# Optimization experiments

Hardware: AMD Instinct MI355X
Metric: run time of the kernel (lower is better)

The kernel has to match this reference:

```python
import jax, jax.numpy as jnp
import numpy as np

VOCAB, EMB, H1, H2, T, B = 21, 128, 64, 100, 500, 1024


def lstm(x, W_ih, W_hh, b_ih, b_hh):
    # x: [B, T, D]; torch gate order i, f, g, o
    Bx, H = x.shape[0], W_hh.shape[1]
    xproj = jnp.einsum('btd,gd->btg', x, W_ih) + b_ih  # [B, T, 4H]

    def step(carry, xt):
        h, c = carry
        gates = xt + h @ W_hh.T + b_hh
        i, f, g, o = jnp.split(gates, 4, axis=-1)
        c = jax.nn.sigmoid(f) * c + jax.nn.sigmoid(i) * jnp.tanh(g)
        h = jax.nn.sigmoid(o) * jnp.tanh(c)
        return (h, c), h

    h0 = jnp.zeros((Bx, H), x.dtype)
    _, hs = jax.lax.scan(step, (h0, h0), xproj.transpose(1, 0, 2))
    return hs.transpose(1, 0, 2)  # [B, T, H]


def setup_inputs() -> dict:
    key = jax.random.key(0)
    ks = jax.random.split(key, 12)
    s = 0.05
    x_idx = jax.random.randint(ks[0], (B, T), 0, VOCAB, dtype=jnp.int32)
    emb_table = jax.random.normal(ks[1], (VOCAB, EMB), jnp.float32) * s
    emb_table = emb_table.at[0].set(0.0)  # padding_idx=0
    d = dict(
        x_idx=x_idx,
        emb_table=emb_table,
        W_ih1=jax.random.normal(ks[2], (4 * H1, EMB), jnp.float32) * s,
        W_hh1=jax.random.normal(ks[3], (4 * H1, H1), jnp.float32) * s,
        b_ih1=jax.random.normal(ks[4], (4 * H1,), jnp.float32) * s,
        b_hh1=jax.random.normal(ks[5], (4 * H1,), jnp.float32) * s,
        W_ih2=jax.random.normal(ks[6], (4 * H2, H1), jnp.float32) * s,
        W_hh2=jax.random.normal(ks[7], (4 * H2, H2), jnp.float32) * s,
        b_ih2=jax.random.normal(ks[8], (4 * H2,), jnp.float32) * s,
        b_hh2=jax.random.normal(ks[9], (4 * H2,), jnp.float32) * s,
        fc_w=jax.random.normal(ks[10], (1, H2), jnp.float32) * s,
        fc_b=jax.random.normal(ks[11], (1,), jnp.float32) * s,
    )
    return d


def reference(x_idx, emb_table, W_ih1, W_hh1, b_ih1, b_hh1,
              W_ih2, W_hh2, b_ih2, b_hh2, fc_w, fc_b):
    # embedding with padding_idx=0 (row is zero; mask keeps grads faithful)
    x = emb_table[x_idx] * (x_idx != 0)[..., None].astype(emb_table.dtype)  # [B,T,128]
    x = lstm(x, W_ih1, W_hh1, b_ih1, b_hh1)  # [B,T,64]
    # MaxPool1d(kernel=5, stride=5) over time
    Bx, Tx, D = x.shape
    Tp = Tx // 5
    x = x[:, :Tp * 5].reshape(Bx, Tp, 5, D).max(axis=2)  # [B,T/5,64]
    x = lstm(x, W_ih2, W_hh2, b_ih2, b_hh2)  # [B,T/5,100]
    h = x[:, -1, :]
    return jax.nn.sigmoid(h @ fc_w.T + fc_b)  # [B,1]
```

## Files before the change

kernel.cpp:

```cpp
#include <hip/hip_runtime.h>

#define VOCAB 21
#define EMB 128
#define H1 64
#define H2 100
#define T1 500
#define TP 100
#define NB 1024
#define TBL_LD 260
#define LOG2E 1.44269504f

typedef __attribute__((ext_vector_type(8))) short bf16x8;
typedef __attribute__((ext_vector_type(4))) float f32x4;

__device__ __forceinline__ unsigned short f2bf(float x){
    union { float f; unsigned u; } v; v.f = x;
    return (unsigned short)((v.u + 0x8000u) >> 16);
}
__device__ __forceinline__ void bar_lds(){
    asm volatile("s_waitcnt lgkmcnt(0)\n\ts_barrier" ::: "memory");
}
__device__ __forceinline__ float ex2(float x){ return __builtin_amdgcn_exp2f(x); }
__device__ __forceinline__ float rcp(float x){ return __builtin_amdgcn_rcpf(x); }

__global__ void k_table(const float* __restrict__ Wih, const float* __restrict__ emb,
                        const float* __restrict__ bih, const float* __restrict__ bhh,
                        float* __restrict__ table){
    const int p = threadIdx.x;
    const int v = blockIdx.x;
    const int orig = (p & 3) * H1 + (p >> 2);
    float s = bih[orig] + bhh[orig];
    if (v != 0){
        const float* w = Wih + orig * EMB;
        const float* e = emb + v * EMB;
        #pragma unroll 16
        for (int d = 0; d < EMB; ++d) s += w[d]*e[d];
    }
    table[v*TBL_LD + p] = s * LOG2E;
}

__global__ __launch_bounds__(1024, 1) void k_lstm1(
    const int* __restrict__ xidx, const float* __restrict__ Whh,
    const float* __restrict__ tbl_g, unsigned short* __restrict__ x2b){
  __shared__ __align__(16) float table[VOCAB*TBL_LD];
  __shared__ __align__(16) unsigned short hbuf[2][16*64];
  __shared__ int idxs[16*T1];

  const int tid = threadIdx.x;
  const int gt = tid >> 6, l = tid & 63;
  const int b0 = blockIdx.x * 16;
  const int row = l & 15, kg = l >> 4;

  for (int i = tid; i < VOCAB*TBL_LD; i += 1024) table[i] = tbl_g[i];
  for (int i = tid; i < 16*T1; i += 1024){
      int r = i / T1, t = i - r*T1;
      idxs[i] = xidx[(b0 + r)*T1 + t];
  }
  { unsigned short* hz = (unsigned short*)hbuf;
    for (int i = tid; i < 2048; i += 1024) hz[i] = 0; }

  bf16x8 af0, af1;
  {
      const int p = 16*gt + row;
      const int orig = (p & 3)*H1 + (p >> 2);
      bf16x8 f;
      const float* s0 = Whh + orig*H1 + kg*8;
      #pragma unroll
      for (int j = 0; j < 8; ++j) f[j] = (short)f2bf(s0[j] * LOG2E);
      af0 = f;
      const float* s1 = Whh + orig*H1 + 32 + kg*8;
      #pragma unroll
      for (int j = 0; j < 8; ++j) f[j] = (short)f2bf(s1[j] * LOG2E);
      af1 = f;
  }

  char* hb = (char*)hbuf;
  const int swz = (row & 7) << 4;
  const int rb0 = (row*128 + 16*kg) ^ swz;
  const int rb1 = (row*128 + 64 + 16*kg) ^ swz;
  const int cell = 4*gt + kg;
  const int wbh  = (row*128 + 2*cell) ^ swz;
  const float twoL = 2.0f * LOG2E;

  float cc = 0.f, pm = -1e30f;
  __syncthreads();

  int vv = idxs[row*T1];
  f32x4 tq = *(const f32x4*)&table[vv*TBL_LD + 4*cell];
  int vnext = idxs[row*T1 + 1];

  int rp = 0, tm = 0, tp = 0;
  for (int t = 0; t < T1; ++t){
      bf16x8 bf0 = *(const bf16x8*)(hb + rp + rb0);
      bf16x8 bf1 = *(const bf16x8*)(hb + rp + rb1);
      f32x4 a = __builtin_amdgcn_mfma_f32_16x16x32_bf16(af0, bf0, tq, 0,0,0);
      f32x4 z = __builtin_amdgcn_mfma_f32_16x16x32_bf16(af1, bf1, a, 0,0,0);
      f32x4 tqn = *(const f32x4*)&table[vnext*TBL_LD + 4*cell];
      int vn2 = idxs[row*T1 + ((t + 2 < T1) ? (t + 2) : 0)];
      float si = rcp(1.f + ex2(-z[0]));
      float sf = rcp(1.f + ex2(-z[1]));
      float so = rcp(1.f + ex2(-z[3]));
      float tg = 1.f - 2.f*rcp(1.f + ex2(z[2] + z[2]));
      cc = sf*cc + si*tg;
      float th = 1.f - 2.f*rcp(1.f + ex2(twoL*cc));
      float h = so*th;
      const int wp = rp ^ 2048;
      *(unsigned short*)(hb + wp + wbh) = f2bf(h);
      pm = fmaxf(pm, h);
      if (++tm == 5){
          x2b[(b0 + row)*(TP*H1) + tp*H1 + cell] = f2bf(pm);
          pm = -1e30f; tm = 0; ++tp;
      }
      tq = tqn; vnext = vn2;
      rp = wp;
      bar_lds();
  }
}

__global__ __launch_bounds__(512, 1) void k_lstm2(
    const unsigned short* __restrict__ x2b, const float* __restrict__ Wih,
    const float* __restrict__ Whh, const float* __restrict__ bih,
    const float* __restrict__ bhh, const float* __restrict__ fcw,
    const float* __restrict__ fcb, float* __restrict__ out){
  __shared__ __align__(16) unsigned short blds[2][16*128];
  __shared__ float fcred[8][16];

  const int tid = threadIdx.x;
  const int w = tid >> 6, l = tid & 63;
  const int b0 = blockIdx.x * 16;
  const int n = l & 15, kg = l >> 4;
  const int tlo = (w < 2) ? 4*w : 8 + 3*(w - 2);
  const int nt  = (w < 2) ? 4 : 3;

  { unsigned short* bz0 = (unsigned short*)blds;
    for (int i = tid; i < 4096; i += 512) bz0[i] = 0; }

  bf16x8 af[4][6];
  #pragma unroll
  for (int u = 0; u < 4; ++u){
      if (u < nt){
          const int p = 16*(tlo + u) + n;
          const int cell_ = p >> 2, gate = p & 3;
          #pragma unroll
          for (int c = 0; c < 6; ++c){
              bf16x8 f;
              #pragma unroll
              for (int jj = 0; jj < 8; ++jj){
                  int k = c*32 + kg*8 + jj;
                  float vv = 0.f;
                  if (cell_ < H2){
                      if (k < 64)           vv = Wih[(gate*H2 + cell_)*H1 + k];
                      else if (k < 64 + H2) vv = Whh[(gate*H2 + cell_)*H2 + (k - 64)];
                  }
                  f[jj] = (short)f2bf(vv * LOG2E);
              }
              af[u][c] = f;
          }
      }
  }

  f32x4 bz[4];
  int cu[4], wbh[4];
  float fw[4];
  #pragma unroll
  for (int u = 0; u < 4; ++u){
      cu[u] = 4*(tlo + u) + kg;
      f32x4 b = {0.f,0.f,0.f,0.f};
      float fv = 0.f;
      if (u < nt && cu[u] < H2){
          #pragma unroll
          for (int g = 0; g < 4; ++g) b[g] = (bih[g*H2 + cu[u]] + bhh[g*H2 + cu[u]]) * LOG2E;
          fv = fcw[cu[u]];
      }
      bz[u] = b; fw[u] = fv;
      wbh[u] = (n*256 + 2*cu[u]) ^ ((n & 7) << 4);
  }
  const float twoL = 2.0f * LOG2E;

  char* bb = (char*)blds;
  int rbh[4];
  #pragma unroll
  for (int j = 0; j < 4; ++j)
      rbh[j] = (n*256 + 2*(j*32 + 8*kg)) ^ ((n & 7) << 4);

  const unsigned short* xrow = x2b + (b0 + n)*(TP*H1) + kg*8;
  bf16x8 x0 = *(const bf16x8*)(xrow);
  bf16x8 x1 = *(const bf16x8*)(xrow + 32);
  float cc[4] = {0.f,0.f,0.f,0.f};
  float hv[4] = {0.f,0.f,0.f,0.f};
  __syncthreads();

  int rp = 0;
  for (int t = 0; t < TP; ++t){
      bf16x8 xn0, xn1;
      if (t + 1 < TP){
          xn0 = *(const bf16x8*)(xrow + (t+1)*H1);
          xn1 = *(const bf16x8*)(xrow + (t+1)*H1 + 32);
      }
      bf16x8 h0 = *(const bf16x8*)(bb + rp + rbh[0]);
      bf16x8 h1 = *(const bf16x8*)(bb + rp + rbh[1]);
      bf16x8 h2 = *(const bf16x8*)(bb + rp + rbh[2]);
      bf16x8 h3 = *(const bf16x8*)(bb + rp + rbh[3]);
      const int wp = rp ^ 4096;
      #pragma unroll
      for (int u = 0; u < 4; ++u){
          if (u < nt){
              f32x4 za = __builtin_amdgcn_mfma_f32_16x16x32_bf16(af[u][0], x0, bz[u], 0,0,0);
              f32x4 zb = __builtin_amdgcn_mfma_f32_16x16x32_bf16(af[u][1], x1, (f32x4){0.f,0.f,0.f,0.f}, 0,0,0);
              za = __builtin_amdgcn_mfma_f32_16x16x32_bf16(af[u][2], h0, za, 0,0,0);
              zb = __builtin_amdgcn_mfma_f32_16x16x32_bf16(af[u][3], h1, zb, 0,0,0);
              za = __builtin_amdgcn_mfma_f32_16x16x32_bf16(af[u][4], h2, za, 0,0,0);
              zb = __builtin_amdgcn_mfma_f32_16x16x32_bf16(af[u][5], h3, zb, 0,0,0);
              f32x4 z = za + zb;
              float si = rcp(1.f + ex2(-z[0]));
              float sf = rcp(1.f + ex2(-z[1]));
              float so = rcp(1.f + ex2(-z[3]));
              float tg = 1.f - 2.f*rcp(1.f + ex2(z[2] + z[2]));
              cc[u] = sf*cc[u] + si*tg;
              float th = 1.f - 2.f*rcp(1.f + ex2(twoL*cc[u]));
              hv[u] = so*th;
              if (cu[u] < H2)
                  *(unsigned short*)(bb + wp + wbh[u]) = f2bf(hv[u]);
          }
      }
      x0 = xn0; x1 = xn1;
      rp = wp;
      bar_lds();
  }

  float p = 0.f;
  #pragma unroll
  for (int u = 0; u < 4; ++u)
      if (u < nt && cu[u] < H2) p += hv[u] * fw[u];
  p += __shfl_xor(p, 16);
  p += __shfl_xor(p, 32);
  if (l < 16) fcred[w][l] = p;
  __syncthreads();
  if (tid < 16){
      float s = 0.f;
      #pragma unroll
      for (int ww = 0; ww < 8; ++ww) s += fcred[ww][tid];
      s += fcb[0];
      out[b0 + tid] = rcp(1.f + ex2(-s * LOG2E));
  }
}

extern "C" void kernel_launch(void* const* d_in, const int* in_sizes, int n_in,
                              void* d_out, int out_size, void* d_ws, size_t ws_size,
                              hipStream_t stream) {
    const int*   x_idx = (const int*)  d_in[0];
    const float* emb   = (const float*)d_in[1];
    const float* Wih1  = (const float*)d_in[2];
    const float* Whh1  = (const float*)d_in[3];
    const float* bih1  = (const float*)d_in[4];
    const float* bhh1  = (const float*)d_in[5];
    const float* Wih2  = (const float*)d_in[6];
    const float* Whh2  = (const float*)d_in[7];
    const float* bih2  = (const float*)d_in[8];
    const float* bhh2  = (const float*)d_in[9];
    const float* fcw   = (const float*)d_in[10];
    const float* fcb   = (const float*)d_in[11];
    float* out = (float*)d_out;

    float*          table = (float*)d_ws;
    unsigned short* x2b   = (unsigned short*)((char*)d_ws + 32768);

    k_table<<<VOCAB, 256, 0, stream>>>(Wih1, emb, bih1, bhh1, table);
    k_lstm1<<<NB / 16, 1024, 0, stream>>>(x_idx, Whh1, table, x2b);
    k_lstm2<<<NB / 16, 512, 0, stream>>>(x2b, Wih2, Whh2, bih2, bhh2, fcw, fcb, out);
}
```

Baseline: 312.3 us.

## Transpose gate table layout and deepen x prefetch in second LSTM

The precomputed embedding-gate table is stored transposed (gate-major, vocab-minor) so each lane reads four scalars at stride VOCAB instead of one 16-byte vector at stride 260. The aim is to cut LDS bank conflicts in the per-step gather, since different rows hit different vocab entries. The cost is four scalar LDS loads in place of one vector load. The second kernel also prefetches the x input two steps ahead instead of one, to hide global-load latency behind the recurrent loop, at the cost of extra registers.

Result: no change. 316.8 us (+1.5%).

```diff
diff --git a/kernel.cpp b/kernel.cpp
--- a/kernel.cpp
+++ b/kernel.cpp
@@ -7,7 +7,6 @@
 #define T1 500
 #define TP 100
 #define NB 1024
-#define TBL_LD 260
 #define LOG2E 1.44269504f
 
 typedef __attribute__((ext_vector_type(8))) short bf16x8;
@@ -36,13 +35,13 @@
         #pragma unroll 16
         for (int d = 0; d < EMB; ++d) s += w[d]*e[d];
     }
-    table[v*TBL_LD + p] = s * LOG2E;
+    table[p*VOCAB + v] = s * LOG2E;
 }
 
 __global__ __launch_bounds__(1024, 1) void k_lstm1(
     const int* __restrict__ xidx, const float* __restrict__ Whh,
     const float* __restrict__ tbl_g, unsigned short* __restrict__ x2b){
-  __shared__ __align__(16) float table[VOCAB*TBL_LD];
+  __shared__ __align__(16) float table[256*VOCAB];
   __shared__ __align__(16) unsigned short hbuf[2][16*64];
   __shared__ int idxs[16*T1];
 
@@ -51,7 +50,7 @@
   const int b0 = blockIdx.x * 16;
   const int row = l & 15, kg = l >> 4;
 
-  for (int i = tid; i < VOCAB*TBL_LD; i += 1024) table[i] = tbl_g[i];
+  for (int i = tid; i < 256*VOCAB; i += 1024) table[i] = tbl_g[i];
   for (int i = tid; i < 16*T1; i += 1024){
       int r = i / T1, t = i - r*T1;
       idxs[i] = xidx[(b0 + r)*T1 + t];
@@ -81,12 +80,15 @@
   const int cell = 4*gt + kg;
   const int wbh  = (row*128 + 2*cell) ^ swz;
   const float twoL = 2.0f * LOG2E;
+  const float* tb0 = &table[cell*4*VOCAB];
 
   float cc = 0.f, pm = -1e30f;
   __syncthreads();
 
   int vv = idxs[row*T1];
-  f32x4 tq = *(const f32x4*)&table[vv*TBL_LD + 4*cell];
+  f32x4 tq;
+  tq[0] = tb0[vv]; tq[1] = tb0[VOCAB + vv];
+  tq[2] = tb0[2*VOCAB + vv]; tq[3] = tb0[3*VOCAB + vv];
   int vnext = idxs[row*T1 + 1];
 
   int rp = 0, tm = 0, tp = 0;
@@ -95,7 +97,9 @@
       bf16x8 bf1 = *(const bf16x8*)(hb + rp + rb1);
       f32x4 a = __builtin_amdgcn_mfma_f32_16x16x32_bf16(af0, bf0, tq, 0,0,0);
       f32x4 z = __builtin_amdgcn_mfma_f32_16x16x32_bf16(af1, bf1, a, 0,0,0);
-      f32x4 tqn = *(const f32x4*)&table[vnext*TBL_LD + 4*cell];
+      f32x4 tqn;
+      tqn[0] = tb0[vnext]; tqn[1] = tb0[VOCAB + vnext];
+      tqn[2] = tb0[2*VOCAB + vnext]; tqn[3] = tb0[3*VOCAB + vnext];
       int vn2 = idxs[row*T1 + ((t + 2 < T1) ? (t + 2) : 0)];
       float si = rcp(1.f + ex2(-z[0]));
       float sf = rcp(1.f + ex2(-z[1]));
@@ -184,18 +188,20 @@
       rbh[j] = (n*256 + 2*(j*32 + 8*kg)) ^ ((n & 7) << 4);
 
   const unsigned short* xrow = x2b + (b0 + n)*(TP*H1) + kg*8;
-  bf16x8 x0 = *(const bf16x8*)(xrow);
-  bf16x8 x1 = *(const bf16x8*)(xrow + 32);
+  bf16x8 xc0 = *(const bf16x8*)(xrow);
+  bf16x8 xc1 = *(const bf16x8*)(xrow + 32);
+  bf16x8 xA0 = *(const bf16x8*)(xrow + H1);
+  bf16x8 xA1 = *(const bf16x8*)(xrow + H1 + 32);
   float cc[4] = {0.f,0.f,0.f,0.f};
   float hv[4] = {0.f,0.f,0.f,0.f};
   __syncthreads();
 
   int rp = 0;
   for (int t = 0; t < TP; ++t){
-      bf16x8 xn0, xn1;
-      if (t + 1 < TP){
-          xn0 = *(const bf16x8*)(xrow + (t+1)*H1);
-          xn1 = *(const bf16x8*)(xrow + (t+1)*H1 + 32);
+      bf16x8 xB0, xB1;
+      if (t + 2 < TP){
+          xB0 = *(const bf16x8*)(xrow + (t+2)*H1);
+          xB1 = *(const bf16x8*)(xrow + (t+2)*H1 + 32);
       }
       bf16x8 h0 = *(const bf16x8*)(bb + rp + rbh[0]);
       bf16x8 h1 = *(const bf16x8*)(bb + rp + rbh[1]);
@@ -205,8 +211,8 @@
       #pragma unroll
       for (int u = 0; u < 4; ++u){
           if (u < nt){
-              f32x4 za = __builtin_amdgcn_mfma_f32_16x16x32_bf16(af[u][0], x0, bz[u], 0,0,0);
-              f32x4 zb = __builtin_amdgcn_mfma_f32_16x16x32_bf16(af[u][1], x1, (f32x4){0.f,0.f,0.f,0.f}, 0,0,0);
+              f32x4 za = __builtin_amdgcn_mfma_f32_16x16x32_bf16(af[u][0], xc0, bz[u], 0,0,0);
+              f32x4 zb = __builtin_amdgcn_mfma_f32_16x16x32_bf16(af[u][1], xc1, (f32x4){0.f,0.f,0.f,0.f}, 0,0,0);
               za = __builtin_amdgcn_mfma_f32_16x16x32_bf16(af[u][2], h0, za, 0,0,0);
               zb = __builtin_amdgcn_mfma_f32_16x16x32_bf16(af[u][3], h1, zb, 0,0,0);
               za = __builtin_amdgcn_mfma_f32_16x16x32_bf16(af[u][4], h2, za, 0,0,0);
@@ -223,7 +229,7 @@
                   *(unsigned short*)(bb + wp + wbh[u]) = f2bf(hv[u]);
           }
       }
-      x0 = xn0; x1 = xn1;
+      xc0 = xA0; xc1 = xA1; xA0 = xB0; xA1 = xB1;
       rp = wp;
       bar_lds();
   }
```

## Fuse both LSTM layers into one kernel with LDS-resident pooled activations

Applied to the files above, without the earlier changes.

The two LSTM kernels are merged into one 1024-thread kernel. After every five layer-1 timesteps, the max-pooled hidden state is written to a double-buffered LDS array, and all 16 waves immediately run one layer-2 step from it. This removes the global write and read of the pooled intermediate and the second kernel launch. Layer-2 tiles are spread over 16 waves instead of 8, so each wave handles at most two tiles. In exchange, layer-2 work now sits on layer 1's sequential critical path, and the kernel needs more LDS and registers per block.

Result: faster. 289.3 us (median of 2 runs) (-7.3%).

```diff
diff --git a/kernel.cpp b/kernel.cpp
--- a/kernel.cpp
+++ b/kernel.cpp
@@ -39,12 +39,19 @@
     table[v*TBL_LD + p] = s * LOG2E;
 }
 
-__global__ __launch_bounds__(1024, 1) void k_lstm1(
-    const int* __restrict__ xidx, const float* __restrict__ Whh,
-    const float* __restrict__ tbl_g, unsigned short* __restrict__ x2b){
+__global__ __launch_bounds__(1024, 1) void k_fused(
+    const int* __restrict__ xidx, const float* __restrict__ Whh1,
+    const float* __restrict__ tbl_g,
+    const float* __restrict__ Wih2, const float* __restrict__ Whh2,
+    const float* __restrict__ bih2, const float* __restrict__ bhh2,
+    const float* __restrict__ fcw, const float* __restrict__ fcb,
+    float* __restrict__ out){
   __shared__ __align__(16) float table[VOCAB*TBL_LD];
   __shared__ __align__(16) unsigned short hbuf[2][16*64];
+  __shared__ __align__(16) unsigned short pool[2][16*64];
+  __shared__ __align__(16) unsigned short h2buf[2][16*128];
   __shared__ int idxs[16*T1];
+  __shared__ float fcred[16][16];
 
   const int tid = threadIdx.x;
   const int gt = tid >> 6, l = tid & 63;
@@ -58,88 +65,32 @@
   }
   { unsigned short* hz = (unsigned short*)hbuf;
     for (int i = tid; i < 2048; i += 1024) hz[i] = 0; }
+  { unsigned short* hz = (unsigned short*)h2buf;
+    for (int i = tid; i < 4096; i += 1024) hz[i] = 0; }
 
   bf16x8 af0, af1;
   {
       const int p = 16*gt + row;
       const int orig = (p & 3)*H1 + (p >> 2);
       bf16x8 f;
-      const float* s0 = Whh + orig*H1 + kg*8;
+      const float* s0 = Whh1 + orig*H1 + kg*8;
       #pragma unroll
       for (int j = 0; j < 8; ++j) f[j] = (short)f2bf(s0[j] * LOG2E);
       af0 = f;
-      const float* s1 = Whh + orig*H1 + 32 + kg*8;
+      const float* s1 = Whh1 + orig*H1 + 32 + kg*8;
       #pragma unroll
       for (int j = 0; j < 8; ++j) f[j] = (short)f2bf(s1[j] * LOG2E);
       af1 = f;
   }
 
-  char* hb = (char*)hbuf;
-  const int swz = (row & 7) << 4;
-  const int rb0 = (row*128 + 16*kg) ^ swz;
-  const int rb1 = (row*128 + 64 + 16*kg) ^ swz;
-  const int cell = 4*gt + kg;
-  const int wbh  = (row*128 + 2*cell) ^ swz;
-  const float twoL = 2.0f * LOG2E;
-
-  float cc = 0.f, pm = -1e30f;
-  __syncthreads();
-
-  int vv = idxs[row*T1];
-  f32x4 tq = *(const f32x4*)&table[vv*TBL_LD + 4*cell];
-  int vnext = idxs[row*T1 + 1];
-
-  int rp = 0, tm = 0, tp = 0;
-  for (int t = 0; t < T1; ++t){
-      bf16x8 bf0 = *(const bf16x8*)(hb + rp + rb0);
-      bf16x8 bf1 = *(const bf16x8*)(hb + rp + rb1);
-      f32x4 a = __builtin_amdgcn_mfma_f32_16x16x32_bf16(af0, bf0, tq, 0,0,0);
-      f32x4 z = __builtin_amdgcn_mfma_f32_16x16x32_bf16(af1, bf1, a, 0,0,0);
-      f32x4 tqn = *(const f32x4*)&table[vnext*TBL_LD + 4*cell];
-      int vn2 = idxs[row*T1 + ((t + 2 < T1) ? (t + 2) : 0)];
-      float si = rcp(1.f + ex2(-z[0]));
-      float sf = rcp(1.f + ex2(-z[1]));
-      float so = rcp(1.f + ex2(-z[3]));
-      float tg = 1.f - 2.f*rcp(1.f + ex2(z[2] + z[2]));
-      cc = sf*cc + si*tg;
-      float th = 1.f - 2.f*rcp(1.f + ex2(twoL*cc));
-      float h = so*th;
-      const int wp = rp ^ 2048;
-      *(unsigned short*)(hb + wp + wbh) = f2bf(h);
-      pm = fmaxf(pm, h);
-      if (++tm == 5){
-          x2b[(b0 + row)*(TP*H1) + tp*H1 + cell] = f2bf(pm);
-          pm = -1e30f; tm = 0; ++tp;
-      }
-      tq = tqn; vnext = vn2;
-      rp = wp;
-      bar_lds();
-  }
-}
-
-__global__ __launch_bounds__(512, 1) void k_lstm2(
-    const unsigned short* __restrict__ x2b, const float* __restrict__ Wih,
-    const float* __restrict__ Whh, const float* __restrict__ bih,
-    const float* __restrict__ bhh, const float* __restrict__ fcw,
-    const float* __restrict__ fcb, float* __restrict__ out){
-  __shared__ __align__(16) unsigned short blds[2][16*128];
-  __shared__ float fcred[8][16];
-
-  const int tid = threadIdx.x;
-  const int w = tid >> 6, l = tid & 63;
-  const int b0 = blockIdx.x * 16;
-  const int n = l & 15, kg = l >> 4;
-  const int tlo = (w < 2) ? 4*w : 8 + 3*(w - 2);
-  const int nt  = (w < 2) ? 4 : 3;
-
-  { unsigned short* bz0 = (unsigned short*)blds;
-    for (int i = tid; i < 4096; i += 512) bz0[i] = 0; }
-
-  bf16x8 af[4][6];
-  #pragma unroll
-  for (int u = 0; u < 4; ++u){
-      if (u < nt){
-          const int p = 16*(tlo + u) + n;
+  const int nt2  = (gt < 10) ? 2 : 1;
+  const int t2lo = (gt < 10) ? 2*gt : gt + 10;
+
+  bf16x8 af2[2][6];
+  #pragma unroll
+  for (int u = 0; u < 2; ++u){
+      if (u < nt2){
+          const int p = 16*(t2lo + u) + row;
           const int cell_ = p >> 2, gate = p & 3;
           #pragma unroll
           for (int c = 0; c < 6; ++c){
@@ -149,97 +100,130 @@
                   int k = c*32 + kg*8 + jj;
                   float vv = 0.f;
                   if (cell_ < H2){
-                      if (k < 64)           vv = Wih[(gate*H2 + cell_)*H1 + k];
-                      else if (k < 64 + H2) vv = Whh[(gate*H2 + cell_)*H2 + (k - 64)];
+                      if (k < 64)           vv = Wih2[(gate*H2 + cell_)*H1 + k];
+                      else if (k < 64 + H2) vv = Whh2[(gate*H2 + cell_)*H2 + (k - 64)];
                   }
                   f[jj] = (short)f2bf(vv * LOG2E);
               }
-              af[u][c] = f;
+              af2[u][c] = f;
           }
       }
   }
 
-  f32x4 bz[4];
-  int cu[4], wbh[4];
-  float fw[4];
-  #pragma unroll
-  for (int u = 0; u < 4; ++u){
-      cu[u] = 4*(tlo + u) + kg;
+  f32x4 bz2[2];
+  int cu2[2], wbh2[2];
+  float fw2[2];
+  const int swz = (row & 7) << 4;
+  #pragma unroll
+  for (int u = 0; u < 2; ++u){
+      cu2[u] = 4*(t2lo + u) + kg;
       f32x4 b = {0.f,0.f,0.f,0.f};
       float fv = 0.f;
-      if (u < nt && cu[u] < H2){
+      if (u < nt2 && cu2[u] < H2){
           #pragma unroll
-          for (int g = 0; g < 4; ++g) b[g] = (bih[g*H2 + cu[u]] + bhh[g*H2 + cu[u]]) * LOG2E;
-          fv = fcw[cu[u]];
-      }
-      bz[u] = b; fw[u] = fv;
-      wbh[u] = (n*256 + 2*cu[u]) ^ ((n & 7) << 4);
+          for (int g = 0; g < 4; ++g)
+              b[g] = (bih2[g*H2 + cu2[u]] + bhh2[g*H2 + cu2[u]]) * LOG2E;
+          fv = fcw[cu2[u]];
+      }
+      bz2[u] = b; fw2[u] = fv;
+      wbh2[u] = (row*256 + 2*cu2[u]) ^ swz;
   }
   const float twoL = 2.0f * LOG2E;
 
-  char* bb = (char*)blds;
-  int rbh[4];
+  char* hb  = (char*)hbuf;
+  char* pb  = (char*)pool;
+  char* h2b = (char*)h2buf;
+  const int rb0  = (row*128 + 16*kg) ^ swz;
+  const int rb1  = (row*128 + 64 + 16*kg) ^ swz;
+  const int cell1 = 4*gt + kg;
+  const int wbh1 = (row*128 + 2*cell1) ^ swz;
+  int rbh2[4];
   #pragma unroll
   for (int j = 0; j < 4; ++j)
-      rbh[j] = (n*256 + 2*(j*32 + 8*kg)) ^ ((n & 7) << 4);
-
-  const unsigned short* xrow = x2b + (b0 + n)*(TP*H1) + kg*8;
-  bf16x8 x0 = *(const bf16x8*)(xrow);
-  bf16x8 x1 = *(const bf16x8*)(xrow + 32);
-  float cc[4] = {0.f,0.f,0.f,0.f};
-  float hv[4] = {0.f,0.f,0.f,0.f};
+      rbh2[j] = (row*256 + 2*(j*32 + 8*kg)) ^ swz;
+
+  float cc1 = 0.f, pm = -1e30f;
+  float cc2[2] = {0.f, 0.f}, hv2[2] = {0.f, 0.f};
   __syncthreads();
 
-  int rp = 0;
-  for (int t = 0; t < TP; ++t){
-      bf16x8 xn0, xn1;
-      if (t + 1 < TP){
-          xn0 = *(const bf16x8*)(xrow + (t+1)*H1);
-          xn1 = *(const bf16x8*)(xrow + (t+1)*H1 + 32);
-      }
-      bf16x8 h0 = *(const bf16x8*)(bb + rp + rbh[0]);
-      bf16x8 h1 = *(const bf16x8*)(bb + rp + rbh[1]);
-      bf16x8 h2 = *(const bf16x8*)(bb + rp + rbh[2]);
-      bf16x8 h3 = *(const bf16x8*)(bb + rp + rbh[3]);
-      const int wp = rp ^ 4096;
-      #pragma unroll
-      for (int u = 0; u < 4; ++u){
-          if (u < nt){
-              f32x4 za = __builtin_amdgcn_mfma_f32_16x16x32_bf16(af[u][0], x0, bz[u], 0,0,0);
-              f32x4 zb = __builtin_amdgcn_mfma_f32_16x16x32_bf16(af[u][1], x1, (f32x4){0.f,0.f,0.f,0.f}, 0,0,0);
-              za = __builtin_amdgcn_mfma_f32_16x16x32_bf16(af[u][2], h0, za, 0,0,0);
-              zb = __builtin_amdgcn_mfma_f32_16x16x32_bf16(af[u][3], h1, zb, 0,0,0);
-              za = __builtin_amdgcn_mfma_f32_16x16x32_bf16(af[u][4], h2, za, 0,0,0);
-              zb = __builtin_amdgcn_mfma_f32_16x16x32_bf16(af[u][5], h3, zb, 0,0,0);
-              f32x4 z = za + zb;
-              float si = rcp(1.f + ex2(-z[0]));
-              float sf = rcp(1.f + ex2(-z[1]));
-              float so = rcp(1.f + ex2(-z[3]));
-              float tg = 1.f - 2.f*rcp(1.f + ex2(z[2] + z[2]));
-              cc[u] = sf*cc[u] + si*tg;
-              float th = 1.f - 2.f*rcp(1.f + ex2(twoL*cc[u]));
-              hv[u] = so*th;
-              if (cu[u] < H2)
-                  *(unsigned short*)(bb + wp + wbh[u]) = f2bf(hv[u]);
+  int vv = idxs[row*T1];
+  f32x4 tq = *(const f32x4*)&table[vv*TBL_LD + 4*cell1];
+  int vnext = idxs[row*T1 + 1];
+
+  int rp1 = 0, rp2 = 0, t = 0;
+  for (int tp = 0; tp < TP; ++tp){
+      #pragma unroll
+      for (int s = 0; s < 5; ++s, ++t){
+          bf16x8 bf0 = *(const bf16x8*)(hb + rp1 + rb0);
+          bf16x8 bf1 = *(const bf16x8*)(hb + rp1 + rb1);
+          f32x4 a = __builtin_amdgcn_mfma_f32_16x16x32_bf16(af0, bf0, tq, 0,0,0);
+          f32x4 z = __builtin_amdgcn_mfma_f32_16x16x32_bf16(af1, bf1, a, 0,0,0);
+          f32x4 tqn = *(const f32x4*)&table[vnext*TBL_LD + 4*cell1];
+          int vn2 = idxs[row*T1 + ((t + 2 < T1) ? (t + 2) : 0)];
+          float si = rcp(1.f + ex2(-z[0]));
+          float sf = rcp(1.f + ex2(-z[1]));
+          float so = rcp(1.f + ex2(-z[3]));
+          float tg = 1.f - 2.f*rcp(1.f + ex2(z[2] + z[2]));
+          cc1 = sf*cc1 + si*tg;
+          float th = 1.f - 2.f*rcp(1.f + ex2(twoL*cc1));
+          float h = so*th;
+          const int wp1 = rp1 ^ 2048;
+          *(unsigned short*)(hb + wp1 + wbh1) = f2bf(h);
+          pm = fmaxf(pm, h);
+          if (s == 4){
+              *(unsigned short*)(pb + ((tp & 1) ? 2048 : 0) + wbh1) = f2bf(pm);
+              pm = -1e30f;
           }
-      }
-      x0 = xn0; x1 = xn1;
-      rp = wp;
-      bar_lds();
+          tq = tqn; vnext = vn2;
+          rp1 = wp1;
+          bar_lds();
+      }
+      {
+          const int po = (tp & 1) ? 2048 : 0;
+          bf16x8 x0 = *(const bf16x8*)(pb + po + rb0);
+          bf16x8 x1 = *(const bf16x8*)(pb + po + rb1);
+          bf16x8 h0 = *(const bf16x8*)(h2b + rp2 + rbh2[0]);
+          bf16x8 h1 = *(const bf16x8*)(h2b + rp2 + rbh2[1]);
+          bf16x8 h2 = *(const bf16x8*)(h2b + rp2 + rbh2[2]);
+          bf16x8 h3 = *(const bf16x8*)(h2b + rp2 + rbh2[3]);
+          const int wp2 = rp2 ^ 4096;
+          #pragma unroll
+          for (int u = 0; u < 2; ++u){
+              if (u < nt2){
+                  f32x4 za = __builtin_amdgcn_mfma_f32_16x16x32_bf16(af2[u][0], x0, bz2[u], 0,0,0);
+                  f32x4 zb = __builtin_amdgcn_mfma_f32_16x16x32_bf16(af2[u][1], x1, (f32x4){0.f,0.f,0.f,0.f}, 0,0,0);
+                  za = __builtin_amdgcn_mfma_f32_16x16x32_bf16(af2[u][2], h0, za, 0,0,0);
+                  zb = __builtin_amdgcn_mfma_f32_16x16x32_bf16(af2[u][3], h1, zb, 0,0,0);
+                  za = __builtin_amdgcn_mfma_f32_16x16x32_bf16(af2[u][4], h2, za, 0,0,0);
+                  zb = __builtin_amdgcn_mfma_f32_16x16x32_bf16(af2[u][5], h3, zb, 0,0,0);
+                  f32x4 q = za + zb;
+                  float si = rcp(1.f + ex2(-q[0]));
+                  float sf = rcp(1.f + ex2(-q[1]));
+                  float so = rcp(1.f + ex2(-q[3]));
+                  float tg = 1.f - 2.f*rcp(1.f + ex2(q[2] + q[2]));
+                  cc2[u] = sf*cc2[u] + si*tg;
+                  float th = 1.f - 2.f*rcp(1.f + ex2(twoL*cc2[u]));
+                  hv2[u] = so*th;
+                  if (cu2[u] < H2)
+                      *(unsigned short*)(h2b + wp2 + wbh2[u]) = f2bf(hv2[u]);
+              }
+          }
+          rp2 = wp2;
+      }
   }
 
   float p = 0.f;
   #pragma unroll
-  for (int u = 0; u < 4; ++u)
-      if (u < nt && cu[u] < H2) p += hv[u] * fw[u];
+  for (int u = 0; u < 2; ++u)
+      if (u < nt2 && cu2[u] < H2) p += hv2[u] * fw2[u];
   p += __shfl_xor(p, 16);
   p += __shfl_xor(p, 32);
-  if (l < 16) fcred[w][l] = p;
+  if (l < 16) fcred[gt][l] = p;
   __syncthreads();
   if (tid < 16){
       float s = 0.f;
       #pragma unroll
-      for (int ww = 0; ww < 8; ++ww) s += fcred[ww][tid];
+      for (int ww = 0; ww < 16; ++ww) s += fcred[ww][tid];
       s += fcb[0];
       out[b0 + tid] = rcp(1.f + ex2(-s * LOG2E));
   }
@@ -262,10 +246,10 @@
     const float* fcb   = (const float*)d_in[11];
     float* out = (float*)d_out;
 
-    float*          table = (float*)d_ws;
-    unsigned short* x2b   = (unsigned short*)((char*)d_ws + 32768);
+    float* table = (float*)d_ws;
 
     k_table<<<VOCAB, 256, 0, stream>>>(Wih1, emb, bih1, bhh1, table);
-    k_lstm1<<<NB / 16, 1024, 0, stream>>>(x_idx, Whh1, table, x2b);
-    k_lstm2<<<NB / 16, 512, 0, stream>>>(x2b, Wih2, Whh2, bih2, bhh2, fcw, fcb, out);
-}
+    k_fused<<<NB / 16, 1024, 0, stream>>>(x_idx, Whh1, table,
+                                          Wih2, Whh2, bih2, bhh2,
+                                          fcw, fcb, out);
+}
```
